# Optimization experiments

Hardware: AMD Instinct MI355X
Metric: run time of the kernel (lower is better)

## Reference

```python
import jax, jax.numpy as jnp
import numpy as np

SEGMENT_LENGTHS = [2048, 4096, 8192]
DILATION_RATES = [1, 2, 4]
BATCH, SEQ_LEN, HEADS, HEAD_DIM = 1, 8192, 16, 64
SCALE = HEAD_DIM ** (-0.5)


def _hilbert_index_to_xy(index, n):
    # Exact replica of the torch module's integer Hilbert d->(x,y) mapping.
    x = y = 0
    s = 1
    while s < n:
        rx = 1 & (index // 2)
        ry = 1 & (index ^ rx)
        if ry == 0:
            if rx == 1:
                x, y = s - 1 - y, s - 1 - x
            x, y = y, x
        x += s * rx
        y += s * ry
        index //= 4
        s *= 2
    return x, y


def _hilbert_perm(n):
    # Replicates _generate_hilbert_indices, including the fill-in tail and
    d = 1
    while d * d < n:
        d *= 2
    idx = []
    for i in range(min(n, d * d)):
        x, y = _hilbert_index_to_xy(i, d)
        p = x * d + y
        if p < n:
            idx.append(p)
    if len(idx) < n:
        idx.extend(range(len(idx), n))
    perm = np.array(idx[:n], dtype=np.int64)
    inv = np.zeros(n, dtype=np.int64)
    inv[perm] = np.arange(n, dtype=np.int64)
    return perm, inv


_PERM_CACHE = {}


def _get_perm(n):
    if n not in _PERM_CACHE:
        _PERM_CACHE[n] = _hilbert_perm(n)
    return _PERM_CACHE[n]


def setup_inputs() -> dict:
    key = jax.random.key(0)
    kq, kk, kv = jax.random.split(key, 3)
    shape = (BATCH, SEQ_LEN, HEADS, HEAD_DIM)
    return {
        "q": jax.random.normal(kq, shape, dtype=jnp.float32),
        "k": jax.random.normal(kk, shape, dtype=jnp.float32),
        "v": jax.random.normal(kv, shape, dtype=jnp.float32),
    }


def reference(q, k, v) -> jnp.ndarray:
    B, L, H, D = q.shape
    n_groups = len(SEGMENT_LENGTHS)
    heads_per_group = max(1, H // n_groups)
    out = jnp.zeros_like(q)
    for g, (seg_len, dil) in enumerate(zip(SEGMENT_LENGTHS, DILATION_RATES)):
        S = min(seg_len, L)
        h0 = g * heads_per_group
        if h0 >= H:
            continue
        h1 = min(h0 + heads_per_group, H)
        assert L % S == 0, "seq_len must tile into segments"
        N = L // S  # number of segments
        Hg = h1 - h0
        # [B, N, S, Hg, D]
        qg = q[:, :, h0:h1].reshape(B, N, S, Hg, D)
        kg = k[:, :, h0:h1].reshape(B, N, S, Hg, D)
        vg = v[:, :, h0:h1].reshape(B, N, S, Hg, D)
        if S > 64:
            perm, inv = _get_perm(S)
        else:
            perm = np.arange(S, dtype=np.int64)
            inv = perm
        # dilation applied AFTER Hilbert ordering -> compose the gathers
        kv_idx = perm[np.arange(0, S, dil)]
        qp = qg[:, :, perm]           # [B,N,S,Hg,D]
        kd = kg[:, :, kv_idx]         # [B,N,S/dil,Hg,D]
        vd = vg[:, :, kv_idx]
        scores = jnp.einsum('bnqhd,bnkhd->bnhqk', qp, kd) * SCALE
        attn = jnp.nan_to_num(jax.nn.softmax(scores, axis=-1))
        og = jnp.einsum('bnhqk,bnkhd->bnqhd', attn, vd)  # [B,N,S,Hg,D]
        og = og[:, :, inv]            # inverse Hilbert scatter
        out = out.at[:, :, h0:h1].set(og.reshape(B, L, Hg, D))
    return out
```

## Files before the change

kernel.cpp:

```cpp
#include <hip/hip_runtime.h>
#include <hip/hip_bf16.h>

typedef __attribute__((ext_vector_type(8))) short bf16x8;
typedef __attribute__((ext_vector_type(4))) short s16x4;
typedef __attribute__((ext_vector_type(4))) float f32x4;

#define LDKP 72

__device__ __forceinline__ unsigned pk2(float a, float b) {
    union { __hip_bfloat162 h2; unsigned u; } c;
    c.h2 = __float22bfloat162_rn(make_float2(a, b));
    return c.u;
}

__device__ __forceinline__ void gld16(const void* g, void* l) {
    __builtin_amdgcn_global_load_lds(
        (const __attribute__((address_space(1))) unsigned*)g,
        (__attribute__((address_space(3))) unsigned*)l, 16, 0, 0);
}

__device__ inline int hilbert_p(int index, int d) {
    int x = 0, y = 0;
    for (int s = 1; s < d; s <<= 1) {
        int rx = (index >> 1) & 1;
        int ry = (index ^ rx) & 1;
        if (ry == 0) {
            if (rx == 1) {
                int nx = s - 1 - y;
                int ny = s - 1 - x;
                x = nx; y = ny;
            }
            int t = x; x = y; y = t;
        }
        x += s * rx;
        y += s * ry;
        index >>= 2;
    }
    return x * d + y;
}

__global__ __launch_bounds__(256) void gather_kv(
    const float* __restrict__ K, const float* __restrict__ V,
    short* __restrict__ Kp, short* __restrict__ Vp)
{
    __shared__ short vt[64 * LDKP];

    const int b = blockIdx.x;
    int g, rb;
    if (b < 640)      { g = 0; rb = b; }
    else if (b < 960) { g = 1; rb = b - 640; }
    else              { g = 2; rb = b - 960; }
    const int nseg   = 4 >> g;
    const int hl     = rb / (nseg * 32);
    const int r2     = rb - hl * (nseg * 32);
    const int seg    = r2 >> 5;
    const int kt     = r2 & 31;
    const int h      = g * 5 + hl;
    const int S      = 2048 << g;
    const int segrow = seg * S;
    const int dgrid  = (g == 2) ? 128 : 64;
    const size_t tile_s = (size_t)b * 4096;

    for (int it = threadIdx.x; it < 512; it += 256) {
        const int j  = it >> 3;
        const int c8 = it & 7;
        const int ii = kt * 64 + j;
        const int p  = (g == 0) ? ii : hilbert_p(ii << g, dgrid);
        const size_t src = ((size_t)((segrow + p) * 16 + h)) * 64 + c8 * 8;
        const float4* kp = (const float4*)(K + src);
        const float4* vp = (const float4*)(V + src);
        float4 k0 = kp[0], k1 = kp[1];
        float4 v0 = vp[0], v1 = vp[1];
        union { unsigned u[4]; bf16x8 v; } ck, cv;
        ck.u[0] = pk2(k0.x, k0.y); ck.u[1] = pk2(k0.z, k0.w);
        ck.u[2] = pk2(k1.x, k1.y); ck.u[3] = pk2(k1.z, k1.w);
        cv.u[0] = pk2(v0.x, v0.y); cv.u[1] = pk2(v0.z, v0.w);
        cv.u[2] = pk2(v1.x, v1.y); cv.u[3] = pk2(v1.z, v1.w);
        *(bf16x8*)&Kp[tile_s + j * 64 + ((c8 ^ (j & 7)) * 8)] = ck.v;
        *(bf16x8*)&vt[j * LDKP + c8 * 8] = cv.v;
    }
    __syncthreads();
    for (int it = threadIdx.x; it < 512; it += 256) {
        const int dd = it >> 3;
        const int k8 = it & 7;
        union { short s[8]; bf16x8 v; } o;
#pragma unroll
        for (int u = 0; u < 8; ++u)
            o.s[u] = vt[(k8 * 8 + u) * LDKP + dd];
        *(bf16x8*)&Vp[tile_s + dd * 64 + ((k8 ^ (dd & 7)) * 8)] = o.v;
    }
}

__global__ __launch_bounds__(256, 4) void attn_kernel(
    const float* __restrict__ Q, float* __restrict__ O,
    const short* __restrict__ Kp, const short* __restrict__ Vp)
{
    __shared__ __align__(16) short ldsK[4096];
    __shared__ __align__(16) short ldsV[4096];
    __shared__ __align__(16) short ldsP[128 * LDKP];

    const int bx = blockIdx.x;
    const int g  = bx / 320;
    const int r  = bx - g * 320;
    const int hl = r >> 6;
    const int qb = r & 63;
    const int h  = g * 5 + hl;
    const int qglob = qb * 128;
    const int seg   = qb >> (4 + g);
    const int tile0 = ((g == 0) ? 0 : (g == 1) ? 640 : 960) + (hl * (4 >> g) + seg) * 32;

    const int tid  = threadIdx.x;
    const int wave = tid >> 6;
    const int lane = tid & 63;
    const int ln   = lane & 15;
    const int quad = lane >> 4;

    if (g == 0 && hl == 0) {
        const float4 z = make_float4(0.f, 0.f, 0.f, 0.f);
        for (int i = tid; i < 2048; i += 256) {
            int row = qglob + (i >> 4);
            ((float4*)O)[(size_t)(row * 16 + 15) * 16 + (i & 15)] = z;
        }
    }

    const float cs = 0.125f * 1.44269504088896f;
    bf16x8 qf[2][2];
#pragma unroll
    for (int m2 = 0; m2 < 2; ++m2) {
        int qrow = qglob + wave * 32 + m2 * 16 + ln;
        const float* qp = Q + ((size_t)(qrow * 16 + h)) * 64;
#pragma unroll
        for (int kh = 0; kh < 2; ++kh) {
            const float4* p4 = (const float4*)(qp + kh * 32 + quad * 8);
            float4 a = p4[0], b = p4[1];
            union { unsigned u[4]; bf16x8 v; } f;
            f.u[0] = pk2(a.x * cs, a.y * cs); f.u[1] = pk2(a.z * cs, a.w * cs);
            f.u[2] = pk2(b.x * cs, b.y * cs); f.u[3] = pk2(b.z * cs, b.w * cs);
            qf[m2][kh] = f.v;
        }
    }

    f32x4 oacc[2][4];
#pragma unroll
    for (int a = 0; a < 2; ++a)
#pragma unroll
        for (int b = 0; b < 4; ++b)
            oacc[a][b] = (f32x4){0.f, 0.f, 0.f, 0.f};
    float lp[2] = {0.f, 0.f};

    for (int kt = 0; kt < 32; ++kt) {
        __syncthreads();
        {
            const size_t tb = (size_t)(tile0 + kt) << 13;
            const char* kgp = (const char*)Kp + tb + (wave << 11) + (lane << 4);
            const char* vgp = (const char*)Vp + tb + (wave << 11) + (lane << 4);
            char* klp = (char*)ldsK + (wave << 11);
            char* vlp = (char*)ldsV + (wave << 11);
            gld16(kgp,        klp);
            gld16(kgp + 1024, klp + 1024);
            gld16(vgp,        vlp);
            gld16(vgp + 1024, vlp + 1024);
        }
        __syncthreads();

        bf16x8 kf[4][2];
#pragma unroll
        for (int kg = 0; kg < 4; ++kg)
#pragma unroll
            for (int kh = 0; kh < 2; ++kh)
                kf[kg][kh] = *(const bf16x8*)&ldsK[(kg * 16 + ln) * 64 + (((kh * 4 + quad) ^ (ln & 7)) * 8)];

#pragma unroll
        for (int m2 = 0; m2 < 2; ++m2) {
            float lacc = 0.f;
#pragma unroll
            for (int kg = 0; kg < 4; ++kg) {
                f32x4 st = (f32x4){0.f, 0.f, 0.f, 0.f};
                st = __builtin_amdgcn_mfma_f32_16x16x32_bf16(kf[kg][0], qf[m2][0], st, 0, 0, 0);
                st = __builtin_amdgcn_mfma_f32_16x16x32_bf16(kf[kg][1], qf[m2][1], st, 0, 0, 0);
                float p0 = __builtin_amdgcn_exp2f(st[0]);
                float p1 = __builtin_amdgcn_exp2f(st[1]);
                float p2 = __builtin_amdgcn_exp2f(st[2]);
                float p3 = __builtin_amdgcn_exp2f(st[3]);
                lacc += (p0 + p1) + (p2 + p3);
                union { unsigned u[2]; s16x4 s; } pc;
                pc.u[0] = pk2(p0, p1); pc.u[1] = pk2(p2, p3);
                *(s16x4*)&ldsP[(wave * 32 + m2 * 16 + ln) * LDKP + kg * 16 + quad * 4] = pc.s;
            }
            lp[m2] += lacc;
        }
        __syncthreads();

        bf16x8 vf[4][2];
#pragma unroll
        for (int n4 = 0; n4 < 4; ++n4)
#pragma unroll
            for (int kh = 0; kh < 2; ++kh)
                vf[n4][kh] = *(const bf16x8*)&ldsV[(n4 * 16 + ln) * 64 + (((kh * 4 + quad) ^ (ln & 7)) * 8)];
#pragma unroll
        for (int m2 = 0; m2 < 2; ++m2) {
            const short* prow = &ldsP[(wave * 32 + m2 * 16 + ln) * LDKP];
            bf16x8 ap0 = *(const bf16x8*)(prow + quad * 8);
            bf16x8 ap1 = *(const bf16x8*)(prow + 32 + quad * 8);
#pragma unroll
            for (int n4 = 0; n4 < 4; ++n4) {
                oacc[m2][n4] = __builtin_amdgcn_mfma_f32_16x16x32_bf16(ap0, vf[n4][0], oacc[m2][n4], 0, 0, 0);
                oacc[m2][n4] = __builtin_amdgcn_mfma_f32_16x16x32_bf16(ap1, vf[n4][1], oacc[m2][n4], 0, 0, 0);
            }
        }
    }

    lp[0] += __shfl_xor(lp[0], 16, 64);
    lp[0] += __shfl_xor(lp[0], 32, 64);
    lp[1] += __shfl_xor(lp[1], 16, 64);
    lp[1] += __shfl_xor(lp[1], 32, 64);

#pragma unroll
    for (int m2 = 0; m2 < 2; ++m2) {
#pragma unroll
        for (int rg = 0; rg < 4; ++rg) {
            float lv  = __shfl(lp[m2], quad * 4 + rg, 64);
            float inv = 1.0f / lv;
            int qrow = qglob + wave * 32 + m2 * 16 + quad * 4 + rg;
            float* op = O + ((size_t)(qrow * 16 + h)) * 64;
#pragma unroll
            for (int n4 = 0; n4 < 4; ++n4)
                op[n4 * 16 + ln] = oacc[m2][n4][rg] * inv;
        }
    }
}

extern "C" void kernel_launch(void* const* d_in, const int* in_sizes, int n_in,
                              void* d_out, int out_size, void* d_ws, size_t ws_size,
                              hipStream_t stream) {
    const float* q = (const float*)d_in[0];
    const float* k = (const float*)d_in[1];
    const float* v = (const float*)d_in[2];
    float* out = (float*)d_out;
    short* Kp = (short*)d_ws;
    short* Vp = Kp + (size_t)1120 * 4096;

    gather_kv<<<1120, 256, 0, stream>>>(k, v, Kp, Vp);
    attn_kernel<<<960, 256, 0, stream>>>(q, out, Kp, Vp);
}
```

Baseline: 207.2 us.

## Double-buffer K/V tiles in attention and swizzle V transpose in gather

The attention loop now uses two LDS buffers for K and V. The next tile's async global-to-LDS load is issued before the current tile is computed, and hand-placed s_waitcnt vmcnt plus s_barrier replace the three __syncthreads per iteration. The barrier between writing and reading P is dropped, since each wave only touches its own P rows. s_setprio raises wave priority around the MFMA sections. The gather kernel's V transpose buffer is XOR-swizzled to cut LDS bank conflicts. In exchange, LDS use grows and occupancy drops from 4 to 3 blocks per SM, and the manual wait counts rely on the exact number of outstanding memory operations.

```diff
diff --git a/kernel.cpp b/kernel.cpp
--- a/kernel.cpp
+++ b/kernel.cpp
@@ -77,7 +77,7 @@
         cv.u[0] = pk2(v0.x, v0.y); cv.u[1] = pk2(v0.z, v0.w);
         cv.u[2] = pk2(v1.x, v1.y); cv.u[3] = pk2(v1.z, v1.w);
         *(bf16x8*)&Kp[tile_s + j * 64 + ((c8 ^ (j & 7)) * 8)] = ck.v;
-        *(bf16x8*)&vt[j * LDKP + c8 * 8] = cv.v;
+        *(bf16x8*)&vt[j * LDKP + ((c8 ^ (j >> 3)) * 8)] = cv.v;
     }
     __syncthreads();
     for (int it = threadIdx.x; it < 512; it += 256) {
@@ -86,17 +86,17 @@
         union { short s[8]; bf16x8 v; } o;
 #pragma unroll
         for (int u = 0; u < 8; ++u)
-            o.s[u] = vt[(k8 * 8 + u) * LDKP + dd];
+            o.s[u] = vt[(k8 * 8 + u) * LDKP + (((dd >> 3) ^ k8) * 8) + (dd & 7)];
         *(bf16x8*)&Vp[tile_s + dd * 64 + ((k8 ^ (dd & 7)) * 8)] = o.v;
     }
 }
 
-__global__ __launch_bounds__(256, 4) void attn_kernel(
+__global__ __launch_bounds__(256, 3) void attn_kernel(
     const float* __restrict__ Q, float* __restrict__ O,
     const short* __restrict__ Kp, const short* __restrict__ Vp)
 {
-    __shared__ __align__(16) short ldsK[4096];
-    __shared__ __align__(16) short ldsV[4096];
+    __shared__ __align__(16) short ldsK[2][4096];
+    __shared__ __align__(16) short ldsV[2][4096];
     __shared__ __align__(16) short ldsP[128 * LDKP];
 
     const int bx = blockIdx.x;
@@ -148,28 +148,47 @@
             oacc[a][b] = (f32x4){0.f, 0.f, 0.f, 0.f};
     float lp[2] = {0.f, 0.f};
 
+    {
+        const size_t tb = (size_t)tile0 << 13;
+        const char* kgp = (const char*)Kp + tb + (wave << 11) + (lane << 4);
+        const char* vgp = (const char*)Vp + tb + (wave << 11) + (lane << 4);
+        char* klp = (char*)&ldsK[0][0] + (wave << 11);
+        char* vlp = (char*)&ldsV[0][0] + (wave << 11);
+        gld16(kgp,        klp);
+        gld16(kgp + 1024, klp + 1024);
+        gld16(vgp,        vlp);
+        gld16(vgp + 1024, vlp + 1024);
+    }
+
     for (int kt = 0; kt < 32; ++kt) {
-        __syncthreads();
-        {
-            const size_t tb = (size_t)(tile0 + kt) << 13;
+        const int cur = kt & 1;
+        if (kt < 31) {
+            const size_t tb = (size_t)(tile0 + kt + 1) << 13;
             const char* kgp = (const char*)Kp + tb + (wave << 11) + (lane << 4);
             const char* vgp = (const char*)Vp + tb + (wave << 11) + (lane << 4);
-            char* klp = (char*)ldsK + (wave << 11);
-            char* vlp = (char*)ldsV + (wave << 11);
+            char* klp = (char*)&ldsK[cur ^ 1][0] + (wave << 11);
+            char* vlp = (char*)&ldsV[cur ^ 1][0] + (wave << 11);
             gld16(kgp,        klp);
             gld16(kgp + 1024, klp + 1024);
             gld16(vgp,        vlp);
             gld16(vgp + 1024, vlp + 1024);
-        }
-        __syncthreads();
+            asm volatile("s_waitcnt vmcnt(4)" ::: "memory");
+        } else {
+            asm volatile("s_waitcnt vmcnt(0)" ::: "memory");
+        }
+        asm volatile("s_barrier" ::: "memory");
+
+        const short* lK = ldsK[cur];
+        const short* lV = ldsV[cur];
 
         bf16x8 kf[4][2];
 #pragma unroll
         for (int kg = 0; kg < 4; ++kg)
 #pragma unroll
             for (int kh = 0; kh < 2; ++kh)
-                kf[kg][kh] = *(const bf16x8*)&ldsK[(kg * 16 + ln) * 64 + (((kh * 4 + quad) ^ (ln & 7)) * 8)];
-
+                kf[kg][kh] = *(const bf16x8*)&lK[(kg * 16 + ln) * 64 + (((kh * 4 + quad) ^ (ln & 7)) * 8)];
+
+        __builtin_amdgcn_s_setprio(1);
 #pragma unroll
         for (int m2 = 0; m2 < 2; ++m2) {
             float lacc = 0.f;
@@ -189,14 +208,15 @@
             }
             lp[m2] += lacc;
         }
-        __syncthreads();
+        __builtin_amdgcn_s_setprio(0);
 
         bf16x8 vf[4][2];
 #pragma unroll
         for (int n4 = 0; n4 < 4; ++n4)
 #pragma unroll
             for (int kh = 0; kh < 2; ++kh)
-                vf[n4][kh] = *(const bf16x8*)&ldsV[(n4 * 16 + ln) * 64 + (((kh * 4 + quad) ^ (ln & 7)) * 8)];
+                vf[n4][kh] = *(const bf16x8*)&lV[(n4 * 16 + ln) * 64 + (((kh * 4 + quad) ^ (ln & 7)) * 8)];
+        __builtin_amdgcn_s_setprio(1);
 #pragma unroll
         for (int m2 = 0; m2 < 2; ++m2) {
             const short* prow = &ldsP[(wave * 32 + m2 * 16 + ln) * LDKP];
@@ -208,6 +228,9 @@
                 oacc[m2][n4] = __builtin_amdgcn_mfma_f32_16x16x32_bf16(ap1, vf[n4][1], oacc[m2][n4], 0, 0, 0);
             }
         }
+        __builtin_amdgcn_s_setprio(0);
+
+        asm volatile("s_barrier" ::: "memory");
     }
 
     lp[0] += __shfl_xor(lp[0], 16, 64);
```

After: 222.0 us. 7.1% more time.
